# Optimization experiments

Measured on AMD Instinct MI355X. Metric: run time of the kernel, lower is better.

The kernel has to match this reference:

```python
import jax, jax.numpy as jnp
import numpy as np

N_QUBITS = 4
N_LAYERS = 3
B = 65536
EPS = 1e-5  # BatchNorm1d default eps

CNOT = jnp.array([[1, 0, 0, 0],
                  [0, 1, 0, 0],
                  [0, 0, 0, 1],
                  [0, 0, 1, 0]], dtype=jnp.complex64)


def _apply_1q(state, U, q):
    # state: [B, 2,2,2,2]; U: [2,2] (shared) or [B,2,2] (per-sample)
    s = jnp.moveaxis(state, 1 + q, -1)
    if U.ndim == 3:
        s = jnp.einsum('b...j,bij->b...i', s, U)
    else:
        s = jnp.einsum('...j,ij->...i', s, U)
    return jnp.moveaxis(s, -1, 1 + q)


def _apply_cnot(state, c, t):
    s = jnp.moveaxis(state, (1 + c, 1 + t), (-2, -1))
    shp = s.shape
    s = jnp.einsum('...j,ij->...i', s.reshape(shp[:-2] + (4,)), CNOT)
    return jnp.moveaxis(s.reshape(shp), (-2, -1), (1 + c, 1 + t))


def _rx_batched(theta):  # theta: [B] -> [B,2,2]
    c = jnp.cos(theta / 2).astype(jnp.complex64)
    s = (-1j * jnp.sin(theta / 2).astype(jnp.complex64))
    return jnp.stack([jnp.stack([c, s], -1), jnp.stack([s, c], -1)], -2)


def _ry(theta):  # scalar -> [2,2]
    c = jnp.cos(theta / 2).astype(jnp.complex64)
    s = jnp.sin(theta / 2).astype(jnp.complex64)
    return jnp.stack([jnp.stack([c, -s]), jnp.stack([s, c])])


def _rz(theta):  # scalar -> [2,2] diagonal
    e = jnp.exp(-1j * theta.astype(jnp.complex64) / 2)
    z = jnp.zeros_like(e)
    return jnp.stack([jnp.stack([e, z]), jnp.stack([z, jnp.conj(e)])])


def _circuit(angles, qparams):
    bsz = angles.shape[0]
    state = jnp.zeros((bsz, 2 ** N_QUBITS), jnp.complex64).at[:, 0].set(1.0)
    state = state.reshape((bsz,) + (2,) * N_QUBITS)
    for q in range(N_QUBITS):
        state = _apply_1q(state, _rx_batched(angles[:, q]), q)
    for l in range(N_LAYERS):
        for q in range(N_QUBITS):
            state = _apply_1q(state, _ry(qparams[l, q, 0]), q)
            state = _apply_1q(state, _rz(qparams[l, q, 1]), q)
        for q in range(N_QUBITS - 1):
            state = _apply_cnot(state, q, q + 1)
        state = _apply_cnot(state, N_QUBITS - 1, 0)
    probs = jnp.abs(state) ** 2  # [B,2,2,2,2]
    zs = []
    for q in range(N_QUBITS):
        axes = tuple(a for a in range(1, N_QUBITS + 1) if a != 1 + q)
        p = probs.sum(axes)  # [B,2]
        zs.append(p[:, 0] - p[:, 1])
    return jnp.stack(zs, -1)  # [B, n_qubits]


def setup_inputs() -> dict:
    key = jax.random.key(0)
    k1, k2, k3 = jax.random.split(key, 3)
    x = jax.random.normal(k1, (B, 1, 24, 24), dtype=jnp.float32)
    enc_w = 0.1 * jax.random.normal(k2, (N_QUBITS, 16), dtype=jnp.float32)
    enc_b = jnp.zeros((N_QUBITS,), jnp.float32)
    qparams = 0.01 * jax.random.normal(k3, (N_LAYERS, N_QUBITS, 3), dtype=jnp.float32)
    gamma = jnp.ones((N_QUBITS,), jnp.float32)
    beta = jnp.zeros((N_QUBITS,), jnp.float32)
    return {"x": x, "enc_w": enc_w, "enc_b": enc_b, "qparams": qparams,
            "gamma": gamma, "beta": beta}


def reference(x, enc_w, enc_b, qparams, gamma, beta):
    bsz = x.shape[0]
    # avg_pool2d(kernel=6, stride=6): [B,1,24,24] -> [B,1,4,4] -> [B,16]
    pooled = x.reshape(bsz, 1, 4, 6, 4, 6).mean((3, 5)).reshape(bsz, 16)
    angles = pooled @ enc_w.T + enc_b  # [B, n_qubits]
    out = _circuit(angles, qparams)    # [B, n_qubits]
    # BatchNorm1d (training mode: batch stats, biased var)
    mean = out.mean(0)
    var = out.var(0)
    return (out - mean) / jnp.sqrt(var + EPS) * gamma + beta
```

## Files before the change

### kernel.cpp

```cpp
#include <hip/hip_runtime.h>
#include <math.h>


#define BATCH 65536
#define SPW 8
#define MAIN_BLOCKS (BATCH / (4 * SPW))

__global__ __launch_bounds__(256) void qnat_precompute(const float* __restrict__ qp,
                                                       float* __restrict__ A,
                                                       double* __restrict__ acc) {
  __shared__ float Ur[16][17], Ui[16][17];
  const int tid = threadIdx.x;
  if (tid >= 64 && tid < 72) acc[tid - 64] = 0.0;
  if (tid < 16) {
    const int col = tid;
    float ur[16], ui[16];
#pragma unroll
    for (int i = 0; i < 16; i++) { ur[i] = (i == col) ? 1.f : 0.f; ui[i] = 0.f; }
#pragma unroll
    for (int l = 0; l < 3; l++) {
#pragma unroll
      for (int q = 0; q < 4; q++) {
        const int b = 3 - q;
        const float ty = qp[(l * 4 + q) * 3 + 0];
        const float tz = qp[(l * 4 + q) * 3 + 1];
        const float cy = cosf(0.5f * ty), sy = sinf(0.5f * ty);
#pragma unroll
        for (int i0 = 0; i0 < 16; i0++) {
          if (((i0 >> b) & 1) == 0) {
            const int i1 = i0 | (1 << b);
            const float r0 = ur[i0], m0 = ui[i0], r1 = ur[i1], m1 = ui[i1];
            ur[i0] = cy * r0 - sy * r1;  ui[i0] = cy * m0 - sy * m1;
            ur[i1] = sy * r0 + cy * r1;  ui[i1] = sy * m0 + cy * m1;
          }
        }
        const float cz = cosf(0.5f * tz), sz = sinf(0.5f * tz);
#pragma unroll
        for (int i0 = 0; i0 < 16; i0++) {
          if (((i0 >> b) & 1) == 0) {
            const int i1 = i0 | (1 << b);
            const float r0 = ur[i0], m0 = ui[i0], r1 = ur[i1], m1 = ui[i1];
            ur[i0] = cz * r0 + sz * m0;  ui[i0] = cz * m0 - sz * r0;
            ur[i1] = cz * r1 - sz * m1;  ui[i1] = cz * m1 + sz * r1;
          }
        }
      }
      const int cb[4] = {3, 2, 1, 0};
      const int tb[4] = {2, 1, 0, 3};
#pragma unroll
      for (int e = 0; e < 4; e++) {
#pragma unroll
        for (int i = 0; i < 16; i++) {
          if (((i >> cb[e]) & 1) && (((i >> tb[e]) & 1) == 0)) {
            const int j2 = i | (1 << tb[e]);
            float t0 = ur[i]; ur[i] = ur[j2]; ur[j2] = t0;
            float t1 = ui[i]; ui[i] = ui[j2]; ui[j2] = t1;
          }
        }
      }
    }
#pragma unroll
    for (int i = 0; i < 16; i++) { Ur[i][col] = ur[i]; Ui[i][col] = ui[i]; }
  }
  __syncthreads();
  const int j = tid >> 4, k = tid & 15;
#pragma unroll
  for (int q = 0; q < 4; q++) {
    const int b = 3 - q;
    float mr = 0.f, mi = 0.f;
#pragma unroll
    for (int i = 0; i < 16; i++) {
      const float z = ((i >> b) & 1) ? -1.f : 1.f;
      const float ar = Ur[i][j], ai = Ui[i][j], br = Ur[i][k], bi = Ui[i][k];
      mr += z * (ar * br + ai * bi);
      mi += z * (ar * bi - ai * br);
    }
    const int e = (__popc((unsigned)j) - __popc((unsigned)k)) & 3;
    A[(q << 8) + tid] = (e == 0) ? mr : (e == 1) ? -mi : (e == 2) ? -mr : mi;
  }
}

__global__ __launch_bounds__(256, 4) void qnat_main(const float* __restrict__ x,
                                                    const float* __restrict__ enc_w,
                                                    const float* __restrict__ enc_b,
                                                    const float* __restrict__ A,
                                                    float* __restrict__ out,
                                                    double* __restrict__ acc) {
  __shared__ float4 sW4[16];
  __shared__ double sAcc[4][4][2];
  const int tid = threadIdx.x;
  if (tid < 16) {
    const float inv36 = 1.0f / 36.0f;
    sW4[tid] = make_float4(enc_w[tid] * inv36, enc_w[16 + tid] * inv36,
                           enc_w[32 + tid] * inv36, enc_w[48 + tid] * inv36);
  }
  __syncthreads();

  const int wave = tid >> 6, lane = tid & 63;
  const int j = lane & 15;
  const int g = lane >> 4;
  const bool bit0 = lane & 1, bit1 = lane & 2;

  float4 wXr[3], wYr[3];
#pragma unroll
  for (int t = 0; t < 3; t++) {
    int p0 = t * 256 + 4 * lane;
    if (p0 > 572) p0 = 572;
    const int row = p0 / 24, col = p0 - row * 24;
    const int rr = (row / 6) * 4;
    wXr[t] = sW4[rr + col / 6];
    wYr[t] = sW4[rr + (col + 3) / 6];
  }
  float Areg[16];
#pragma unroll
  for (int k = 0; k < 16; k++) Areg[k] = A[(g << 8) + (j << 4) + k];
  const float bq = enc_b[lane & 3];

  const int s0 = (blockIdx.x * 4 + wave) * SPW;
  double sd = 0.0, ssd = 0.0;

  auto LOADB = [&](float4& V0, float4& V1, float4& V2, int S) {
    if (S > BATCH - 1) S = BATCH - 1;
    const float4* p4 = (const float4*)(x + (size_t)S * 576);
    V0 = p4[lane];
    V1 = p4[64 + lane];
    V2 = (lane < 16) ? p4[128 + lane] : make_float4(0.f, 0.f, 0.f, 0.f);
  };

  auto COMPUTE = [&](const float4& V0, const float4& V1, const float4& V2, int s) {
    float a0 = 0.f, a1 = 0.f, a2 = 0.f, a3 = 0.f;
#define ACCT(V, T)                                           \
    {                                                        \
      const float h0 = V.x + V.y, h1 = V.z + V.w;            \
      a0 = fmaf(h0, wXr[T].x, fmaf(h1, wYr[T].x, a0));       \
      a1 = fmaf(h0, wXr[T].y, fmaf(h1, wYr[T].y, a1));       \
      a2 = fmaf(h0, wXr[T].z, fmaf(h1, wYr[T].z, a2));       \
      a3 = fmaf(h0, wXr[T].w, fmaf(h1, wYr[T].w, a3));       \
    }
    ACCT(V0, 0) ACCT(V1, 1) ACCT(V2, 2)
#undef ACCT
    float snd, rcv;
    snd = bit0 ? a0 : a1; rcv = __shfl_xor(snd, 1);
    float Af = (bit0 ? a1 : a0) + rcv;
    snd = bit0 ? a2 : a3; rcv = __shfl_xor(snd, 1);
    float Bf = (bit0 ? a3 : a2) + rcv;
    snd = bit1 ? Af : Bf; rcv = __shfl_xor(snd, 2);
    float Cf = (bit1 ? Bf : Af) + rcv;
    Cf += __shfl_xor(Cf, 4);
    Cf += __shfl_xor(Cf, 8);
    Cf += __shfl_xor(Cf, 16);
    Cf += __shfl_xor(Cf, 32);

    float sm, cm;
    __sincosf(0.5f * (Cf + bq), &sm, &cm);

    const int base = lane & ~3;
    const float c0 = __shfl(cm, base + 0), s0_ = __shfl(sm, base + 0);
    const float c1 = __shfl(cm, base + 1), s1_ = __shfl(sm, base + 1);
    const float c2 = __shfl(cm, base + 2), s2_ = __shfl(sm, base + 2);
    const float c3 = __shfl(cm, base + 3), s3_ = __shfl(sm, base + 3);

    const float p01[4] = {c0 * c1, c0 * s1_, s0_ * c1, s0_ * s1_};
    const float p23[4] = {c2 * c3, c2 * s3_, s2_ * c3, s2_ * s3_};
    float inner = 0.f;
#pragma unroll
    for (int hi = 0; hi < 4; hi++) {
      float sh = 0.f;
#pragma unroll
      for (int lo = 0; lo < 4; lo++) sh = fmaf(Areg[4 * hi + lo], p23[lo], sh);
      inner = fmaf(p01[hi], sh, inner);
    }
    const float rj = ((j & 8) ? s0_ : c0) * ((j & 4) ? s1_ : c1) *
                     ((j & 2) ? s2_ : c2) * ((j & 1) ? s3_ : c3);
    float v = inner * rj;
    v += __shfl_xor(v, 1);
    v += __shfl_xor(v, 2);
    v += __shfl_xor(v, 4);
    v += __shfl_xor(v, 8);
    if (j == 0) {
      out[(size_t)s * 4 + g] = v;
      sd += (double)v;
      ssd = fma((double)v, (double)v, ssd);
    }
  };

  float4 A0, A1, A2, B0, B1, B2, C0, C1, C2;
  LOADB(A0, A1, A2, s0 + 0);
  LOADB(B0, B1, B2, s0 + 1);
  LOADB(C0, C1, C2, s0 + 2);
  COMPUTE(A0, A1, A2, s0 + 0); LOADB(A0, A1, A2, s0 + 3);
  COMPUTE(B0, B1, B2, s0 + 1); LOADB(B0, B1, B2, s0 + 4);
  COMPUTE(C0, C1, C2, s0 + 2); LOADB(C0, C1, C2, s0 + 5);
  COMPUTE(A0, A1, A2, s0 + 3); LOADB(A0, A1, A2, s0 + 6);
  COMPUTE(B0, B1, B2, s0 + 4); LOADB(B0, B1, B2, s0 + 7);
  COMPUTE(C0, C1, C2, s0 + 5);
  COMPUTE(A0, A1, A2, s0 + 6);
  COMPUTE(B0, B1, B2, s0 + 7);

  if (j == 0) { sAcc[wave][g][0] = sd; sAcc[wave][g][1] = ssd; }
  __syncthreads();
  if (tid < 8) {
    const int q = tid & 3, m = tid >> 2;
    const double t = sAcc[0][q][m] + sAcc[1][q][m] + sAcc[2][q][m] + sAcc[3][q][m];
    atomicAdd(&acc[m * 4 + q], t);
  }
}

__global__ __launch_bounds__(256) void qnat_norm(float* __restrict__ out,
                                                 const double* __restrict__ acc,
                                                 const float* __restrict__ gamma,
                                                 const float* __restrict__ beta) {
  __shared__ float sMean[4], sScale[4], sBeta[4];
  const int tid = threadIdx.x;
  if (tid < 4) {
    const double n = (double)BATCH;
    const double mean = acc[tid] / n;
    const double var = acc[4 + tid] / n - mean * mean;
    const double inv = 1.0 / sqrt(var + 1e-5);
    sMean[tid] = (float)mean;
    sScale[tid] = (float)(gamma[tid] * inv);
    sBeta[tid] = beta[tid];
  }
  __syncthreads();
  const size_t i = (size_t)blockIdx.x * 256 + tid;
  float4 v = ((const float4*)out)[i];
  v.x = (v.x - sMean[0]) * sScale[0] + sBeta[0];
  v.y = (v.y - sMean[1]) * sScale[1] + sBeta[1];
  v.z = (v.z - sMean[2]) * sScale[2] + sBeta[2];
  v.w = (v.w - sMean[3]) * sScale[3] + sBeta[3];
  ((float4*)out)[i] = v;
}

extern "C" void kernel_launch(void* const* d_in, const int* in_sizes, int n_in,
                              void* d_out, int out_size, void* d_ws, size_t ws_size,
                              hipStream_t stream) {
  const float* x       = (const float*)d_in[0];
  const float* enc_w   = (const float*)d_in[1];
  const float* enc_b   = (const float*)d_in[2];
  const float* qparams = (const float*)d_in[3];
  const float* gamma   = (const float*)d_in[4];
  const float* beta    = (const float*)d_in[5];
  float* out = (float*)d_out;

  float* A = (float*)d_ws;
  double* acc = (double*)((char*)d_ws + 4096);

  qnat_precompute<<<1, 256, 0, stream>>>(qparams, A, acc);
  qnat_main<<<MAIN_BLOCKS, 256, 0, stream>>>(x, enc_w, enc_b, A, out, acc);
  qnat_norm<<<256, 256, 0, stream>>>(out, acc, gamma, beta);
}
```

Baseline: 58.53 us.

## Move A matrix and encoder weights to LDS, double-buffer loads, raise occupancy

Moves the per-lane 16-entry A matrix and the pooled encoder weight vectors out of registers into shared memory, which are then read inside the compute loop. The load pipeline drops from triple to double buffering, and launch bounds ask for 8 blocks per SM instead of 4. The aim is to cut register pressure so more waves can be resident to hide global memory latency on this bandwidth-bound kernel. The cost is extra LDS reads per sample and a shallower prefetch depth.

```diff
diff --git a/kernel.cpp b/kernel.cpp
--- a/kernel.cpp
+++ b/kernel.cpp
@@ -80,13 +80,14 @@
   }
 }
 
-__global__ __launch_bounds__(256, 4) void qnat_main(const float* __restrict__ x,
+__global__ __launch_bounds__(256, 8) void qnat_main(const float* __restrict__ x,
                                                     const float* __restrict__ enc_w,
                                                     const float* __restrict__ enc_b,
                                                     const float* __restrict__ A,
                                                     float* __restrict__ out,
                                                     double* __restrict__ acc) {
   __shared__ float4 sW4[16];
+  __shared__ float sA[4][16][17];
   __shared__ double sAcc[4][4][2];
   const int tid = threadIdx.x;
   if (tid < 16) {
@@ -94,33 +95,35 @@
     sW4[tid] = make_float4(enc_w[tid] * inv36, enc_w[16 + tid] * inv36,
                            enc_w[32 + tid] * inv36, enc_w[48 + tid] * inv36);
   }
+#pragma unroll
+  for (int m = 0; m < 4; m++) {
+    const int idx = tid * 4 + m;
+    sA[idx >> 8][(idx >> 4) & 15][idx & 15] = A[idx];
+  }
   __syncthreads();
 
   const int wave = tid >> 6, lane = tid & 63;
   const int j = lane & 15;
   const int g = lane >> 4;
   const bool bit0 = lane & 1, bit1 = lane & 2;
-
-  float4 wXr[3], wYr[3];
+  const float* Arow = &sA[g][j][0];
+
+  int iX[3], iY[3];
 #pragma unroll
   for (int t = 0; t < 3; t++) {
     int p0 = t * 256 + 4 * lane;
     if (p0 > 572) p0 = 572;
     const int row = p0 / 24, col = p0 - row * 24;
     const int rr = (row / 6) * 4;
-    wXr[t] = sW4[rr + col / 6];
-    wYr[t] = sW4[rr + (col + 3) / 6];
-  }
-  float Areg[16];
-#pragma unroll
-  for (int k = 0; k < 16; k++) Areg[k] = A[(g << 8) + (j << 4) + k];
+    iX[t] = rr + col / 6;
+    iY[t] = rr + (col + 3) / 6;
+  }
   const float bq = enc_b[lane & 3];
 
   const int s0 = (blockIdx.x * 4 + wave) * SPW;
   double sd = 0.0, ssd = 0.0;
 
   auto LOADB = [&](float4& V0, float4& V1, float4& V2, int S) {
-    if (S > BATCH - 1) S = BATCH - 1;
     const float4* p4 = (const float4*)(x + (size_t)S * 576);
     V0 = p4[lane];
     V1 = p4[64 + lane];
@@ -131,11 +134,12 @@
     float a0 = 0.f, a1 = 0.f, a2 = 0.f, a3 = 0.f;
 #define ACCT(V, T)                                           \
     {                                                        \
+      const float4 wX = sW4[iX[T]], wY = sW4[iY[T]];         \
       const float h0 = V.x + V.y, h1 = V.z + V.w;            \
-      a0 = fmaf(h0, wXr[T].x, fmaf(h1, wYr[T].x, a0));       \
-      a1 = fmaf(h0, wXr[T].y, fmaf(h1, wYr[T].y, a1));       \
-      a2 = fmaf(h0, wXr[T].z, fmaf(h1, wYr[T].z, a2));       \
-      a3 = fmaf(h0, wXr[T].w, fmaf(h1, wYr[T].w, a3));       \
+      a0 = fmaf(h0, wX.x, fmaf(h1, wY.x, a0));               \
+      a1 = fmaf(h0, wX.y, fmaf(h1, wY.y, a1));               \
+      a2 = fmaf(h0, wX.z, fmaf(h1, wY.z, a2));               \
+      a3 = fmaf(h0, wX.w, fmaf(h1, wY.w, a3));               \
     }
     ACCT(V0, 0) ACCT(V1, 1) ACCT(V2, 2)
 #undef ACCT
@@ -167,7 +171,7 @@
     for (int hi = 0; hi < 4; hi++) {
       float sh = 0.f;
 #pragma unroll
-      for (int lo = 0; lo < 4; lo++) sh = fmaf(Areg[4 * hi + lo], p23[lo], sh);
+      for (int lo = 0; lo < 4; lo++) sh = fmaf(Arow[4 * hi + lo], p23[lo], sh);
       inner = fmaf(p01[hi], sh, inner);
     }
     const float rj = ((j & 8) ? s0_ : c0) * ((j & 4) ? s1_ : c1) *
@@ -184,17 +188,15 @@
     }
   };
 
-  float4 A0, A1, A2, B0, B1, B2, C0, C1, C2;
+  float4 A0, A1, A2, B0, B1, B2;
   LOADB(A0, A1, A2, s0 + 0);
-  LOADB(B0, B1, B2, s0 + 1);
-  LOADB(C0, C1, C2, s0 + 2);
-  COMPUTE(A0, A1, A2, s0 + 0); LOADB(A0, A1, A2, s0 + 3);
-  COMPUTE(B0, B1, B2, s0 + 1); LOADB(B0, B1, B2, s0 + 4);
-  COMPUTE(C0, C1, C2, s0 + 2); LOADB(C0, C1, C2, s0 + 5);
-  COMPUTE(A0, A1, A2, s0 + 3); LOADB(A0, A1, A2, s0 + 6);
-  COMPUTE(B0, B1, B2, s0 + 4); LOADB(B0, B1, B2, s0 + 7);
-  COMPUTE(C0, C1, C2, s0 + 5);
-  COMPUTE(A0, A1, A2, s0 + 6);
+  LOADB(B0, B1, B2, s0 + 1); COMPUTE(A0, A1, A2, s0 + 0);
+  LOADB(A0, A1, A2, s0 + 2); COMPUTE(B0, B1, B2, s0 + 1);
+  LOADB(B0, B1, B2, s0 + 3); COMPUTE(A0, A1, A2, s0 + 2);
+  LOADB(A0, A1, A2, s0 + 4); COMPUTE(B0, B1, B2, s0 + 3);
+  LOADB(B0, B1, B2, s0 + 5); COMPUTE(A0, A1, A2, s0 + 4);
+  LOADB(A0, A1, A2, s0 + 6); COMPUTE(B0, B1, B2, s0 + 5);
+  LOADB(B0, B1, B2, s0 + 7); COMPUTE(A0, A1, A2, s0 + 6);
   COMPUTE(B0, B1, B2, s0 + 7);
 
   if (j == 0) { sAcc[wave][g][0] = sd; sAcc[wave][g][1] = ssd; }
```

Result: slower. 81.12 us (+38.6%).
